# Performance work log

Measured on AMD Instinct MI355X. Metric: run time of the kernel, lower is better.

## Reference

```python
import jax, jax.numpy as jnp
import numpy as np

D_MODEL = 2048; D_STATE = 128; D_CONV = 4; EXPAND = 2
HEADDIM = 64; NGROUPS = 1; CHUNK = 256
D_INNER = EXPAND * D_MODEL          # 4096
NHEADS = D_INNER // HEADDIM         # 64
HG = NHEADS // NGROUPS              # heads per group
CONV_DIM = D_INNER + 2 * NGROUPS * D_STATE          # 4352
D_IN_PROJ = 2 * D_INNER + 2 * NGROUPS * D_STATE + NHEADS  # 8512
BATCH = 2; SEQLEN = 2048
EPS = 1e-5


def setup_inputs() -> dict:
    ks = jax.random.split(jax.random.key(0), 8)
    u = jax.random.normal(ks[0], (BATCH, SEQLEN, D_MODEL), jnp.float32)
    in_proj_w = jax.random.normal(ks[1], (D_IN_PROJ, D_MODEL), jnp.float32) * D_MODEL ** -0.5
    conv_w = jax.random.normal(ks[2], (CONV_DIM, D_CONV), jnp.float32) * D_CONV ** -0.5
    conv_b = jax.random.normal(ks[3], (CONV_DIM,), jnp.float32) * 0.1
    # dt_bias init exactly as in the module: inv softplus of dt ~ U(log(1e-3), log(1e-1))
    dt = jnp.exp(jax.random.uniform(ks[4], (NHEADS,), jnp.float32)
                 * (np.float32(np.log(0.1)) - np.float32(np.log(0.001))) + np.float32(np.log(0.001)))
    dt = jnp.clip(dt, 1e-4, None)
    dt_bias = dt + jnp.log(-jnp.expm1(-dt))
    A_log = jnp.log(jax.random.uniform(ks[5], (NHEADS,), jnp.float32, minval=1.0, maxval=16.0))
    D_skip = jnp.ones((NHEADS,), jnp.float32)
    norm_w = jnp.ones((D_INNER,), jnp.float32)
    out_proj_w = jax.random.normal(ks[6], (D_MODEL, D_INNER), jnp.float32) * D_INNER ** -0.5
    return dict(u=u, in_proj_w=in_proj_w, conv_w=conv_w, conv_b=conv_b,
                dt_bias=dt_bias, A_log=A_log, D_skip=D_skip,
                norm_w=norm_w, out_proj_w=out_proj_w)


def _mamba2(u, in_proj_w, conv_w, conv_b, dt_bias, A_log, D_skip, norm_w, out_proj_w):
    b, l, _ = u.shape
    nc = l // CHUNK
    zxbcdt = u @ in_proj_w.T                                   # (b,l,d_in_proj)
    z = zxbcdt[..., :D_INNER]                                  # gate
    xBC = zxbcdt[..., D_INNER:D_INNER + CONV_DIM]
    dt = jax.nn.softplus(zxbcdt[..., D_INNER + CONV_DIM:] + dt_bias)  # (b,l,h)
    # causal depthwise conv1d (padding d_conv-1, truncated to seqlen) + SiLU
    xp = jnp.pad(xBC, ((0, 0), (D_CONV - 1, 0), (0, 0)))
    conv = conv_b + sum(conv_w[:, k] * xp[:, k:k + l, :] for k in range(D_CONV))
    xBC = jax.nn.silu(conv)
    x = xBC[..., :D_INNER].reshape(b, l, NHEADS, HEADDIM)
    Bm = xBC[..., D_INNER:D_INNER + NGROUPS * D_STATE].reshape(b, l, NGROUPS, D_STATE)
    Cm = xBC[..., D_INNER + NGROUPS * D_STATE:].reshape(b, l, NGROUPS, D_STATE)
    A = -jnp.exp(A_log)                                        # (h,)
    # ---- SSD chunked scan ----
    xc = x.reshape(b, nc, CHUNK, NGROUPS, HG, HEADDIM)         # (b,c,s,g,H,p)
    dtc = dt.reshape(b, nc, CHUNK, NGROUPS, HG)                # (b,c,s,g,H)
    Bc = Bm.reshape(b, nc, CHUNK, NGROUPS, D_STATE)            # (b,c,s,g,n)
    Cc = Cm.reshape(b, nc, CHUNK, NGROUPS, D_STATE)
    dA = jnp.transpose(dtc * A.reshape(NGROUPS, HG), (0, 3, 4, 1, 2))  # (b,g,H,c,s)
    dA_cs = jnp.cumsum(dA, axis=-1)                            # (b,g,H,c,s)
    # intra-chunk: L[i,j] = exp(sum_{j<k<=i} dA_k), lower-triangular (diag=1)
    seg = dA_cs[..., :, None] - dA_cs[..., None, :]            # (b,g,H,c,l,s)
    tri = jnp.tril(jnp.ones((CHUNK, CHUNK), bool))
    Lmat = jnp.where(tri, jnp.exp(seg), 0.0)
    xdt = xc * dtc[..., None]                                  # (b,c,s,g,H,p)
    CB = jnp.einsum('bclgn,bcsgn->bcgls', Cc, Bc)
    Y_diag = jnp.einsum('bcgls,bgHcls,bcsgHp->bclgHp', CB, Lmat, xdt)
    # chunk states and inter-chunk recurrence
    decay_states = jnp.exp(dA_cs[..., -1:] - dA_cs)            # (b,g,H,c,s)
    states = jnp.einsum('bcsgn,bgHcs,bcsgHp->bcgHpn', Bc, decay_states, xdt)
    chunk_decay = jnp.exp(dA_cs[..., -1])                      # (b,g,H,c)

    def step(carry, inp):
        st, dec = inp
        return carry * dec[..., None, None] + st, carry

    _, prev = jax.lax.scan(step, jnp.zeros_like(states[:, 0]),
                           (jnp.moveaxis(states, 1, 0), jnp.moveaxis(chunk_decay, -1, 0)))
    prev = jnp.moveaxis(prev, 0, 1)                            # (b,c,g,H,p,n) state entering chunk
    Y_off = jnp.einsum('bclgn,bcgHpn,bgHcl->bclgHp', Cc, prev, jnp.exp(dA_cs))
    y = (Y_diag + Y_off).reshape(b, l, NHEADS, HEADDIM) + x * D_skip[None, None, :, None]
    y = y.reshape(b, l, D_INNER)
    # gated RMSNorm: gate first (norm_before_gate=False), groupwise rms (ngroups=1 -> full)
    y = y * jax.nn.silu(z)
    yg = y.reshape(b, l, NGROUPS, D_INNER // NGROUPS)
    yg = yg * jax.lax.rsqrt(jnp.mean(yg * yg, axis=-1, keepdims=True) + EPS)
    y = yg.reshape(b, l, D_INNER) * norm_w
    return y @ out_proj_w.T                                    # (b,l,d_model)


def reference(u, in_proj_w, conv_w, conv_b, dt_bias, A_log, D_skip, norm_w, out_proj_w):
    return _mamba2(u, in_proj_w, conv_w, conv_b, dt_bias, A_log, D_skip, norm_w, out_proj_w)
```

## Files before the change

### kernel.cpp

```cpp
#include <hip/hip_runtime.h>
#include <hip/hip_bf16.h>


#define D_MODEL   2048
#define D_STATE   128
#define HEADDIM   64
#define CHUNK     256
#define D_INNER   4096
#define NHEADS    64
#define CONV_DIM  4352
#define D_IN_PROJ 8512
#define SEQLEN    2048
#define NC        8
#define ROWSTOT   4096
#define NPAD      8576
#define RMS_EPS   1e-5f

#define OFF_WIN   0ull
#define OFF_XBF   0ull
#define OFF_PREV  0ull
#define OFF_WOUT  16777216ull
#define OFF_UBF   35127296ull
#define OFF_DTV   35127296ull
#define OFF_DACS  36175872ull
#define OFF_BBF   37224448ull
#define OFF_CBF   38273024ull
#define OFF_CB    39321600ull
#define OFF_BT    43515904ull
#define OFF_XBC   51904512ull
#define OFF_STATE 51904512ull
#define OFF_ZBF   87556096ull
#define OFF_DTRAW 121110528ull
#define OFF_YBUF  121110528ull
#define WS_NEEDED 154664960ull

#define N4_U    2097152l
#define N4_WIN  4390912l

typedef __hip_bfloat16 bf16;
typedef __bf16 bfrag8 __attribute__((ext_vector_type(8)));
typedef float  f32x4v __attribute__((ext_vector_type(4)));

__device__ __forceinline__ f32x4v mfma16(bfrag8 a, bfrag8 b, f32x4v c) {
  return __builtin_amdgcn_mfma_f32_16x16x32_bf16(a, b, c, 0, 0, 0);
}

__device__ __forceinline__ void gload_lds16(const void* g, void* l) {
  __builtin_amdgcn_global_load_lds((const __attribute__((address_space(1))) void*)g,
                                   (__attribute__((address_space(3))) void*)l, 16, 0, 0);
}

__device__ __forceinline__ bf16 f2b(float x) { return __float2bfloat16(x); }
__device__ __forceinline__ float b2f(bf16 x) { return __bfloat162float(x); }
__device__ __forceinline__ float siluf(float x) { return x / (1.f + __expf(-x)); }

__global__ __launch_bounds__(256) void cast_all_kernel(const float* __restrict__ u,
    const float* __restrict__ w_in,
    bf16* __restrict__ u_bf, bf16* __restrict__ win_bf) {
  long i = (long)blockIdx.x * 256 + threadIdx.x;
  if (i < N4_U) {
    float4 v = ((const float4*)u)[i];
    bf16* o = u_bf + i * 4;
    o[0] = f2b(v.x); o[1] = f2b(v.y); o[2] = f2b(v.z); o[3] = f2b(v.w);
  } else if (i < N4_U + N4_WIN) {
    long e = (i - N4_U) * 4;
    long row = e / D_MODEL;
    bf16* o = win_bf + e;
    if (row < D_IN_PROJ) {
      float4 v = *(const float4*)(w_in + e);
      o[0] = f2b(v.x); o[1] = f2b(v.y); o[2] = f2b(v.z); o[3] = f2b(v.w);
    } else {
      bf16 z = f2b(0.f);
      o[0] = z; o[1] = z; o[2] = z; o[3] = z;
    }
  }
}


__global__ __launch_bounds__(512) void gemm1_kernel(const bf16* __restrict__ A,
                                                    const bf16* __restrict__ B,
                                                    bf16* __restrict__ zb,
                                                    bf16* __restrict__ xbc,
                                                    float* __restrict__ dtraw) {
  int pid = blockIdx.x;
  int t = pid & 63, s = pid >> 6;
  int sm = s / 9, sn = s % 9;
  int xcd = t & 7, j8 = t >> 3;
  int tm = sm * 8 + (xcd >> 1) * 2 + (j8 & 1);
  int tn = sn * 8 + (xcd & 1) * 4 + (j8 >> 1);
  if (tn >= 67) return;
  long row0 = (long)tm * 256, col0 = (long)tn * 128;

  __shared__ __align__(16) bf16 As[2 * 256 * 32];
  __shared__ __align__(16) bf16 Bs[2 * 128 * 32];
  int tid = threadIdx.x, lane = tid & 63, w = tid >> 6;
  int wr = w >> 1, wc = w & 1, r16 = lane & 15, q = lane >> 4;
  int qs = (q ^ ((r16 >> 1) & 3)) * 8;
  const int K = D_MODEL;
  f32x4v zero4 = {0.f, 0.f, 0.f, 0.f};
  f32x4v acc[4][4];
#pragma unroll
  for (int i = 0; i < 4; ++i)
#pragma unroll
    for (int j = 0; j < 4; ++j) acc[i][j] = zero4;

  for (int kt = 0; kt < K; kt += 64) {
    __syncthreads();
#pragma unroll
    for (int j = 0; j < 4; ++j) {
      int ci = j * 512 + tid;
      int half = ci >> 10, cj = ci & 1023;
      int r = cj >> 2;
      int ko = half * 32 + ((cj & 3) ^ ((cj >> 3) & 3)) * 8;
      gload_lds16(A + (row0 + r) * (long)K + kt + ko,
                  (char*)As + j * 8192 + w * 1024);
    }
#pragma unroll
    for (int j = 0; j < 2; ++j) {
      int ci = j * 512 + tid;
      int half = ci >> 9, cj = ci & 511;
      int r = cj >> 2;
      int ko = half * 32 + ((cj & 3) ^ ((cj >> 3) & 3)) * 8;
      gload_lds16(B + (col0 + r) * (long)K + kt + ko,
                  (char*)Bs + j * 8192 + w * 1024);
    }
    __syncthreads();
#pragma unroll
    for (int ks = 0; ks < 2; ++ks) {
      const bf16* Ab = As + ks * 8192;
      const bf16* Bb = Bs + ks * 4096;
      bfrag8 af[4], bfv[4];
#pragma unroll
      for (int i = 0; i < 4; ++i) af[i]  = *(const bfrag8*)(Ab + (wr * 64 + i * 16 + r16) * 32 + qs);
#pragma unroll
      for (int i = 0; i < 4; ++i) bfv[i] = *(const bfrag8*)(Bb + (wc * 64 + i * 16 + r16) * 32 + qs);
#pragma unroll
      for (int i = 0; i < 4; ++i)
#pragma unroll
        for (int j = 0; j < 4; ++j) acc[i][j] = mfma16(af[i], bfv[j], acc[i][j]);
    }
  }
#pragma unroll
  for (int i = 0; i < 4; ++i)
#pragma unroll
    for (int j = 0; j < 4; ++j) {
      long col = col0 + wc * 64 + j * 16 + r16;
#pragma unroll
      for (int r = 0; r < 4; ++r) {
        long row = row0 + wr * 64 + i * 16 + q * 4 + r;
        float v = acc[i][j][r];
        if (col < D_INNER)                       zb[row * D_INNER + col] = f2b(v);
        else if (col < D_INNER + CONV_DIM)       xbc[row * CONV_DIM + (col - D_INNER)] = f2b(v);
        else if (col < D_IN_PROJ)                dtraw[row * NHEADS + (col - D_INNER - CONV_DIM)] = v;
      }
    }
}

__global__ __launch_bounds__(256) void gemm2_kernel(const bf16* __restrict__ A,
                                                    const bf16* __restrict__ B,
                                                    float* __restrict__ C) {
  int pid = blockIdx.x;
  int t = pid & 63, s = pid >> 6;
  int sm = s >> 1, sn = s & 1;
  int xcd = t & 7, j8 = t >> 3;
  int tm = sm * 8 + (xcd >> 1) * 2 + (j8 & 1);
  int tn = sn * 8 + (xcd & 1) * 4 + (j8 >> 1);
  long row0 = (long)tm * 128, col0 = (long)tn * 128;

  __shared__ __align__(16) bf16 As[2 * 128 * 32];
  __shared__ __align__(16) bf16 Bs[2 * 128 * 32];
  int tid = threadIdx.x, lane = tid & 63, w = tid >> 6;
  int wr = w >> 1, wc = w & 1, r16 = lane & 15, q = lane >> 4;
  int qs = (q ^ ((r16 >> 1) & 3)) * 8;
  const int K = D_INNER, ldc = D_MODEL;
  f32x4v zero4 = {0.f, 0.f, 0.f, 0.f};
  f32x4v acc[4][4];
#pragma unroll
  for (int i = 0; i < 4; ++i)
#pragma unroll
    for (int j = 0; j < 4; ++j) acc[i][j] = zero4;

  for (int kt = 0; kt < K; kt += 64) {
    __syncthreads();
#pragma unroll
    for (int j = 0; j < 4; ++j) {
      int ci = (j * 4 + w) * 64 + lane;
      int half = ci >> 9, cj = ci & 511;
      int r = cj >> 2;
      int ko = half * 32 + ((cj & 3) ^ ((cj >> 3) & 3)) * 8;
      gload_lds16(A + (row0 + r) * (long)K + kt + ko,
                  (char*)As + (j * 4 + w) * 1024);
    }
#pragma unroll
    for (int j = 0; j < 4; ++j) {
      int ci = (j * 4 + w) * 64 + lane;
      int half = ci >> 9, cj = ci & 511;
      int r = cj >> 2;
      int ko = half * 32 + ((cj & 3) ^ ((cj >> 3) & 3)) * 8;
      gload_lds16(B + (col0 + r) * (long)K + kt + ko,
                  (char*)Bs + (j * 4 + w) * 1024);
    }
    __syncthreads();
#pragma unroll
    for (int ks = 0; ks < 2; ++ks) {
      const bf16* Ab = As + ks * 4096;
      const bf16* Bb = Bs + ks * 4096;
      bfrag8 af[4], bfv[4];
#pragma unroll
      for (int i = 0; i < 4; ++i) af[i]  = *(const bfrag8*)(Ab + (wr * 64 + i * 16 + r16) * 32 + qs);
#pragma unroll
      for (int i = 0; i < 4; ++i) bfv[i] = *(const bfrag8*)(Bb + (wc * 64 + i * 16 + r16) * 32 + qs);
#pragma unroll
      for (int i = 0; i < 4; ++i)
#pragma unroll
        for (int j = 0; j < 4; ++j) acc[i][j] = mfma16(af[i], bfv[j], acc[i][j]);
    }
  }
#pragma unroll
  for (int i = 0; i < 4; ++i)
#pragma unroll
    for (int j = 0; j < 4; ++j)
#pragma unroll
      for (int r = 0; r < 4; ++r) {
        long row = row0 + wr * 64 + i * 16 + q * 4 + r;
        long col = col0 + wc * 64 + j * 16 + r16;
        C[row * ldc + col] = acc[i][j][r];
      }
}

__global__ __launch_bounds__(256) void conv_dt_kernel(
    const float* __restrict__ dtraw, const float* __restrict__ dt_bias,
    const float* __restrict__ A_log, float* __restrict__ dtv_buf,
    float* __restrict__ dacs_buf,
    const bf16* __restrict__ xbc, const float* __restrict__ conv_w,
    const float* __restrict__ conv_b, bf16* __restrict__ xo,
    bf16* __restrict__ Bo, bf16* __restrict__ Co, bf16* __restrict__ BT) {
  if (blockIdx.x < 1024) {
    int blk = blockIdx.x;
    int c = blk & 7, h = (blk >> 3) & 63, b = blk >> 9;
    int s = threadIdx.x, lane = s & 63, w = s >> 6;
    long row = (long)b * SEQLEN + c * CHUNK + s;
    float raw = dtraw[row * NHEADS + h] + dt_bias[h];
    float dtv = fmaxf(raw, 0.f) + log1pf(__expf(-fabsf(raw)));
    float A = -__expf(A_log[h]);
    float x = dtv * A;
#pragma unroll
    for (int off = 1; off < 64; off <<= 1) {
      float y = __shfl_up(x, off);
      if (lane >= off) x += y;
    }
    __shared__ __align__(16) float wsum[4];
    if (lane == 63) wsum[w] = x;
    __syncthreads();
    float pre = 0.f;
#pragma unroll
    for (int i = 0; i < 4; ++i) pre += (i < w) ? wsum[i] : 0.f;
    long o = ((long)(b * NHEADS + h) * NC + c) * CHUNK + s;
    dtv_buf[o] = dtv;
    dacs_buf[o] = x + pre;
    return;
  }
  int t = blockIdx.x - 1024;
  int bx = t % 17;
  int rest = t / 17;
  int by = rest & 255, bz = rest >> 8;
  int cidx = bx * 256 + threadIdx.x;
  int l0 = by * 8, b = bz;
  float4 wv = *(const float4*)(conv_w + cidx * 4);
  float bias = conv_b[cidx];
  const bf16* base = xbc + (long)b * SEQLEN * CONV_DIM + cidx;
  float win[11];
#pragma unroll
  for (int k = 0; k < 11; ++k) {
    int ls = l0 - 3 + k;
    win[k] = (ls >= 0) ? b2f(base[(long)ls * CONV_DIM]) : 0.f;
  }
  int cgrp = (cidx < D_INNER) ? 0 : ((cidx < D_INNER + D_STATE) ? 1 : 2);
  int n = cidx - D_INNER;
  int n2 = cidx - D_INNER - D_STATE;
  int cch = l0 >> 8;
#pragma unroll
  for (int j = 0; j < 8; ++j) {
    float acc = bias + wv.x * win[j] + wv.y * win[j + 1] + wv.z * win[j + 2] + wv.w * win[j + 3];
    bf16 o = f2b(siluf(acc));
    int l = l0 + j;
    long rowo = (long)b * SEQLEN + l;
    if (cgrp == 0) {
      xo[rowo * D_INNER + cidx] = o;
    } else if (cgrp == 1) {
      Bo[rowo * D_STATE + n] = o;
      BT[(((long)b * NC + cch) * D_STATE + n) * CHUNK + (l & 255)] = o;
    } else {
      Co[rowo * D_STATE + n2] = o;
    }
  }
}

__global__ __launch_bounds__(256) void cb_kernel(const bf16* __restrict__ Cg,
                                                 const bf16* __restrict__ Bg,
                                                 float* __restrict__ CB) {
  int blk = blockIdx.x;
  int stile = blk & 3, bc = blk >> 2;
  int c = bc & 7, b = bc >> 3;
  int tid = threadIdx.x, lane = tid & 63, w = tid >> 6, r16 = lane & 15, q = lane >> 4;
  const bf16* Cb = Cg + ((long)b * SEQLEN + c * CHUNK) * D_STATE;
  const bf16* Bb = Bg + ((long)b * SEQLEN + c * CHUNK) * D_STATE;
  bfrag8 af[4][4];
#pragma unroll
  for (int lt = 0; lt < 4; ++lt)
#pragma unroll
    for (int kk = 0; kk < 4; ++kk)
      af[lt][kk] = *(const bfrag8*)(Cb + (long)(w * 64 + lt * 16 + r16) * D_STATE + kk * 32 + q * 8);
  float* CBb = CB + (long)bc * CHUNK * CHUNK;
  f32x4v zero4 = {0.f, 0.f, 0.f, 0.f};
  for (int st = stile * 4; st < stile * 4 + 4; ++st) {
    f32x4v acc[4] = {zero4, zero4, zero4, zero4};
#pragma unroll
    for (int kk = 0; kk < 4; ++kk) {
      bfrag8 bfv = *(const bfrag8*)(Bb + (long)(st * 16 + r16) * D_STATE + kk * 32 + q * 8);
#pragma unroll
      for (int lt = 0; lt < 4; ++lt) acc[lt] = mfma16(af[lt][kk], bfv, acc[lt]);
    }
#pragma unroll
    for (int lt = 0; lt < 4; ++lt)
#pragma unroll
      for (int r = 0; r < 4; ++r)
        CBb[(long)(w * 64 + lt * 16 + q * 4 + r) * CHUNK + st * 16 + r16] = acc[lt][r];
  }
}

__global__ __launch_bounds__(256) void ssm_diag_kernel(
    const bf16* __restrict__ xg, const bf16* __restrict__ BT,
    const float* __restrict__ CB, const float* __restrict__ dtv_buf,
    const float* __restrict__ dacs_buf, const float* __restrict__ Dskip,
    bf16* __restrict__ ybuf, float* __restrict__ states) {
  int blk = blockIdx.x;
  int h = blk & 63, cc = (blk >> 6) & 7, b = blk >> 9;
  int tid = threadIdx.x, lane = tid & 63, w = tid >> 6, r16 = lane & 15, q = lane >> 4;

  __shared__ __align__(16) __bf16 xT[HEADDIM][264];
  __shared__ __align__(16) float cs_s[CHUNK];
  __shared__ __align__(16) float dt_s[CHUNK];
  __shared__ __align__(16) float w_s[CHUNK];

  long hco = ((long)(b * NHEADS + h) * NC + cc) * CHUNK;
  cs_s[tid] = dacs_buf[hco + tid];
  dt_s[tid] = dtv_buf[hco + tid];
  __syncthreads();
  float cl_last = cs_s[CHUNK - 1];
  w_s[tid] = __expf(cl_last - cs_s[tid]) * dt_s[tid];

  const __bf16* xbase = (const __bf16*)(xg + ((long)b * SEQLEN + cc * CHUNK) * D_INNER + h * HEADDIM);
#pragma unroll
  for (int it = 0; it < 8; ++it) {
    int e = it * 256 + tid;
    int s = e >> 3, p0 = (e & 7) * 8;
    bfrag8 xv = *(const bfrag8*)(xbase + (long)s * D_INNER + p0);
#pragma unroll
    for (int j = 0; j < 8; ++j) xT[p0 + j][s] = xv[j];
  }
  __syncthreads();

  const float* CBchunk = CB + (long)(b * NC + cc) * CHUNK * CHUNK;
  const __bf16* BTc = (const __bf16*)(BT + (((long)b * NC + cc) * D_STATE) * CHUNK);
  f32x4v zero4 = {0.f, 0.f, 0.f, 0.f};
  f32x4v accY[4][4], accS[2][4];
#pragma unroll
  for (int i = 0; i < 4; ++i)
#pragma unroll
    for (int j = 0; j < 4; ++j) accY[i][j] = zero4;
#pragma unroll
  for (int i = 0; i < 2; ++i)
#pragma unroll
    for (int j = 0; j < 4; ++j) accS[i][j] = zero4;

  int l_row[4];
  const float* CBrow[4];
#pragma unroll
  for (int lt = 0; lt < 4; ++lt) {
    l_row[lt] = w * 64 + lt * 16 + r16;
    CBrow[lt] = CBchunk + (long)l_row[lt] * CHUNK;
  }

#pragma unroll 2
  for (int ks = 0; ks < 8; ++ks) {
    int s0 = ks * 32 + q * 8;
    float4 cs0 = *(const float4*)(cs_s + s0);
    float4 cs1 = *(const float4*)(cs_s + s0 + 4);
    float4 dt0 = *(const float4*)(dt_s + s0);
    float4 dt1 = *(const float4*)(dt_s + s0 + 4);
    float4 w0  = *(const float4*)(w_s + s0);
    float4 w1  = *(const float4*)(w_s + s0 + 4);
    float csv[8] = {cs0.x, cs0.y, cs0.z, cs0.w, cs1.x, cs1.y, cs1.z, cs1.w};
    float dtv8[8] = {dt0.x, dt0.y, dt0.z, dt0.w, dt1.x, dt1.y, dt1.z, dt1.w};
    float wv8[8]  = {w0.x, w0.y, w0.z, w0.w, w1.x, w1.y, w1.z, w1.w};

    bfrag8 xf[4];
#pragma unroll
    for (int pt = 0; pt < 4; ++pt) xf[pt] = *(const bfrag8*)(&xT[pt * 16 + r16][s0]);

#pragma unroll
    for (int lt = 0; lt < 4; ++lt) {
      int l = l_row[lt];
      float cs_l = cs_s[l];
      float4 cb0 = *(const float4*)(CBrow[lt] + s0);
      float4 cb1 = *(const float4*)(CBrow[lt] + s0 + 4);
      float cbv[8] = {cb0.x, cb0.y, cb0.z, cb0.w, cb1.x, cb1.y, cb1.z, cb1.w};
      bfrag8 pf;
#pragma unroll
      for (int j = 0; j < 8; ++j) {
        float v = (s0 + j <= l)
                    ? cbv[j] * __expf(fminf(cs_l - csv[j], 0.f)) * dtv8[j]
                    : 0.f;
        pf[j] = (__bf16)v;
      }
#pragma unroll
      for (int pt = 0; pt < 4; ++pt) accY[lt][pt] = mfma16(pf, xf[pt], accY[lt][pt]);
    }

#pragma unroll
    for (int nt = 0; nt < 2; ++nt) {
      int n = w * 32 + nt * 16 + r16;
      bfrag8 braw = *(const bfrag8*)(BTc + (long)n * CHUNK + s0);
      bfrag8 bwf;
#pragma unroll
      for (int j = 0; j < 8; ++j) bwf[j] = (__bf16)((float)braw[j] * wv8[j]);
#pragma unroll
      for (int pt = 0; pt < 4; ++pt) accS[nt][pt] = mfma16(bwf, xf[pt], accS[nt][pt]);
    }
  }

  float dsk = Dskip[h];
  bf16* ybase = ybuf + ((long)b * SEQLEN + cc * CHUNK) * D_INNER + h * HEADDIM;
#pragma unroll
  for (int lt = 0; lt < 4; ++lt)
#pragma unroll
    for (int pt = 0; pt < 4; ++pt)
#pragma unroll
      for (int r = 0; r < 4; ++r) {
        int lrow = w * 64 + lt * 16 + q * 4 + r;
        int pcol = pt * 16 + r16;
        ybase[(long)lrow * D_INNER + pcol] = f2b(accY[lt][pt][r] + (float)xT[pcol][lrow] * dsk);
      }
  float* sbase = states + (long)blk * (HEADDIM * D_STATE);
#pragma unroll
  for (int nt = 0; nt < 2; ++nt)
#pragma unroll
    for (int pt = 0; pt < 4; ++pt)
#pragma unroll
      for (int r = 0; r < 4; ++r)
        sbase[(long)(pt * 16 + r16) * D_STATE + w * 32 + nt * 16 + q * 4 + r] = accS[nt][pt][r];
}

__global__ __launch_bounds__(256) void state_scan_kernel(const float* __restrict__ states,
    const float* __restrict__ dacs, bf16* __restrict__ prevb) {
  int gid = blockIdx.x;
  int et = gid & 31, bh = gid >> 5;
  int h = bh & 63, b = bh >> 6;
  int e = et * 256 + threadIdx.x;
  float dec[NC];
#pragma unroll
  for (int c = 0; c < NC; ++c)
    dec[c] = __expf(dacs[((long)(b * NHEADS + h) * NC + c) * CHUNK + (CHUNK - 1)]);
  float carry = 0.f;
#pragma unroll
  for (int c = 0; c < NC; ++c) {
    long off = ((long)((b * NC + c) * NHEADS + h)) * (HEADDIM * D_STATE) + e;
    prevb[off] = f2b(carry);
    carry = carry * dec[c] + states[off];
  }
}

__global__ __launch_bounds__(256) void yoff_kernel(const bf16* __restrict__ Cg,
    const bf16* __restrict__ prevb, const float* __restrict__ dacs,
    bf16* __restrict__ ybuf) {
  int blk = blockIdx.x;
  int h = blk & 63, cc = (blk >> 6) & 7, b = blk >> 9;
  int tid = threadIdx.x, lane = tid & 63, w = tid >> 6, r16 = lane & 15, q = lane >> 4;
  __shared__ __align__(16) float cs_s[CHUNK];
  cs_s[tid] = dacs[((long)(b * NHEADS + h) * NC + cc) * CHUNK + tid];
  __syncthreads();
  const bf16* Cb = Cg + ((long)b * SEQLEN + cc * CHUNK) * D_STATE;
  const bf16* Pb = prevb + (long)blk * (HEADDIM * D_STATE);
  f32x4v zero4 = {0.f, 0.f, 0.f, 0.f};
  f32x4v acc[4][4];
#pragma unroll
  for (int i = 0; i < 4; ++i)
#pragma unroll
    for (int j = 0; j < 4; ++j) acc[i][j] = zero4;
#pragma unroll
  for (int kk = 0; kk < 4; ++kk) {
    bfrag8 bv[4];
#pragma unroll
    for (int pt = 0; pt < 4; ++pt)
      bv[pt] = *(const bfrag8*)(Pb + (long)(pt * 16 + r16) * D_STATE + kk * 32 + q * 8);
#pragma unroll
    for (int lt = 0; lt < 4; ++lt) {
      bfrag8 av = *(const bfrag8*)(Cb + (long)(w * 64 + lt * 16 + r16) * D_STATE + kk * 32 + q * 8);
#pragma unroll
      for (int pt = 0; pt < 4; ++pt) acc[lt][pt] = mfma16(av, bv[pt], acc[lt][pt]);
    }
  }
  bf16* ybase = ybuf + ((long)b * SEQLEN + cc * CHUNK) * D_INNER + h * HEADDIM;
#pragma unroll
  for (int lt = 0; lt < 4; ++lt)
#pragma unroll
    for (int pt = 0; pt < 4; ++pt)
#pragma unroll
      for (int r = 0; r < 4; ++r) {
        int lrow = w * 64 + lt * 16 + q * 4 + r;
        float ef = __expf(cs_s[lrow]);
        bf16* p = ybase + (long)lrow * D_INNER + pt * 16 + r16;
        *p = f2b(b2f(*p) + acc[lt][pt][r] * ef);
      }
}

__global__ __launch_bounds__(256) void cast_gate_kernel(
    const float* __restrict__ w_out, bf16* __restrict__ wout_bf,
    bf16* __restrict__ ybuf, const bf16* __restrict__ zb,
    const float* __restrict__ norm_w) {
  if (blockIdx.x < 8192) {
    long i = (long)blockIdx.x * 256 + threadIdx.x;
    float4 v = ((const float4*)w_out)[i];
    bf16* o = wout_bf + i * 4;
    o[0] = f2b(v.x); o[1] = f2b(v.y); o[2] = f2b(v.z); o[3] = f2b(v.w);
    return;
  }
  int row = blockIdx.x - 8192, tid = threadIdx.x;
  bf16* y = ybuf + (long)row * D_INNER;
  const bf16* z = zb + (long)row * D_INNER;
  float v[16];
  float ss = 0.f;
#pragma unroll
  for (int i = 0; i < 2; ++i) {
    int e = tid * 16 + i * 8;
    bfrag8 yv = *(const bfrag8*)(y + e);
    bfrag8 zv = *(const bfrag8*)(z + e);
#pragma unroll
    for (int j = 0; j < 8; ++j) {
      float a = (float)yv[j] * siluf((float)zv[j]);
      v[i * 8 + j] = a;
      ss += a * a;
    }
  }
#pragma unroll
  for (int off = 32; off > 0; off >>= 1) ss += __shfl_down(ss, off);
  __shared__ __align__(16) float red[4];
  int lane = tid & 63, w = tid >> 6;
  if (lane == 0) red[w] = ss;
  __syncthreads();
  float tot = red[0] + red[1] + red[2] + red[3];
  float scale = rsqrtf(tot * (1.f / D_INNER) + RMS_EPS);
#pragma unroll
  for (int i = 0; i < 2; ++i) {
    int e = tid * 16 + i * 8;
    float4 w0 = *(const float4*)(norm_w + e);
    float4 w1 = *(const float4*)(norm_w + e + 4);
    bfrag8 o;
    o[0] = (__bf16)(v[i * 8 + 0] * scale * w0.x);
    o[1] = (__bf16)(v[i * 8 + 1] * scale * w0.y);
    o[2] = (__bf16)(v[i * 8 + 2] * scale * w0.z);
    o[3] = (__bf16)(v[i * 8 + 3] * scale * w0.w);
    o[4] = (__bf16)(v[i * 8 + 4] * scale * w1.x);
    o[5] = (__bf16)(v[i * 8 + 5] * scale * w1.y);
    o[6] = (__bf16)(v[i * 8 + 6] * scale * w1.z);
    o[7] = (__bf16)(v[i * 8 + 7] * scale * w1.w);
    *(bfrag8*)(y + e) = o;
  }
}

extern "C" void kernel_launch(void* const* d_in, const int* in_sizes, int n_in,
                              void* d_out, int out_size, void* d_ws, size_t ws_size,
                              hipStream_t stream) {
  if (ws_size < WS_NEEDED) return;

  const float* u       = (const float*)d_in[0];
  const float* w_in    = (const float*)d_in[1];
  const float* conv_w  = (const float*)d_in[2];
  const float* conv_b  = (const float*)d_in[3];
  const float* dt_bias = (const float*)d_in[4];
  const float* A_log   = (const float*)d_in[5];
  const float* Dskip   = (const float*)d_in[6];
  const float* norm_w  = (const float*)d_in[7];
  const float* w_out   = (const float*)d_in[8];
  float* out = (float*)d_out;

  char* ws = (char*)d_ws;
  bf16*  win_bf  = (bf16*)(ws + OFF_WIN);
  bf16*  x_bf    = (bf16*)(ws + OFF_XBF);
  bf16*  prevb   = (bf16*)(ws + OFF_PREV);
  bf16*  wout_bf = (bf16*)(ws + OFF_WOUT);
  bf16*  u_bf    = (bf16*)(ws + OFF_UBF);
  float* dtv     = (float*)(ws + OFF_DTV);
  float* dacs    = (float*)(ws + OFF_DACS);
  bf16*  B_bf    = (bf16*)(ws + OFF_BBF);
  bf16*  C_bf    = (bf16*)(ws + OFF_CBF);
  float* CBb     = (float*)(ws + OFF_CB);
  bf16*  BT_bf   = (bf16*)(ws + OFF_BT);
  bf16*  xbc_bf  = (bf16*)(ws + OFF_XBC);
  float* states  = (float*)(ws + OFF_STATE);
  bf16*  z_bf    = (bf16*)(ws + OFF_ZBF);
  float* dt_raw  = (float*)(ws + OFF_DTRAW);
  bf16*  ybuf    = (bf16*)(ws + OFF_YBUF);

  cast_all_kernel<<<25344, 256, 0, stream>>>(u, w_in, u_bf, win_bf);
  gemm1_kernel<<<1152, 512, 0, stream>>>(u_bf, win_bf, z_bf, xbc_bf, dt_raw);
  conv_dt_kernel<<<9728, 256, 0, stream>>>(dt_raw, dt_bias, A_log, dtv, dacs,
                                           xbc_bf, conv_w, conv_b, x_bf, B_bf, C_bf, BT_bf);
  cb_kernel<<<64, 256, 0, stream>>>(C_bf, B_bf, CBb);
  ssm_diag_kernel<<<1024, 256, 0, stream>>>(x_bf, BT_bf, CBb, dtv, dacs, Dskip, ybuf, states);
  state_scan_kernel<<<4096, 256, 0, stream>>>(states, dacs, prevb);
  yoff_kernel<<<1024, 256, 0, stream>>>(C_bf, prevb, dacs, ybuf);
  cast_gate_kernel<<<12288, 256, 0, stream>>>(w_out, wout_bf, ybuf, z_bf, norm_w);
  gemm2_kernel<<<512, 256, 0, stream>>>(ybuf, wout_bf, out);
}
```

Before: 561.2 us.

## Rewrite input-projection GEMM with 256x256 tiles and software-pipelined LDS prefetch

The in_proj GEMM moves from 256x128 tiles with a plain load/sync/compute loop to 256x256 tiles. Each tile is split into four 128-row halves staged through a double-buffered LDS ring, and the next k-tile is prefetched while MFMAs run. It uses inline ds_read_b128, explicit vmcnt waits, raw s_barrier, setprio around the MFMA bursts, and a new XCD-aware block mapping over 544 blocks. The aim is to hide global-load latency and raise arithmetic intensity per block. In exchange it uses more registers and LDS, and depends on fragile hand-written waitcnt ordering.

```diff
diff --git a/kernel.cpp b/kernel.cpp
--- a/kernel.cpp
+++ b/kernel.cpp
@@ -53,6 +53,16 @@
 __device__ __forceinline__ bf16 f2b(float x) { return __float2bfloat16(x); }
 __device__ __forceinline__ float b2f(bf16 x) { return __bfloat162float(x); }
 __device__ __forceinline__ float siluf(float x) { return x / (1.f + __expf(-x)); }
+
+#define BARRIER() asm volatile("s_barrier" ::: "memory")
+#define WAITV(N) asm volatile("s_waitcnt vmcnt(" #N ")" ::: "memory")
+
+__device__ __forceinline__ bfrag8 ds_read_b128f(const bf16* p) {
+  bfrag8 d;
+  unsigned a = (unsigned)(unsigned long long)p;
+  asm volatile("ds_read_b128 %0, %1" : "=&v"(d) : "v"(a));
+  return d;
+}
 
 __global__ __launch_bounds__(256) void cast_all_kernel(const float* __restrict__ u,
     const float* __restrict__ w_in,
@@ -77,78 +87,126 @@
 }
 
 
-__global__ __launch_bounds__(512) void gemm1_kernel(const bf16* __restrict__ A,
-                                                    const bf16* __restrict__ B,
-                                                    bf16* __restrict__ zb,
-                                                    bf16* __restrict__ xbc,
-                                                    float* __restrict__ dtraw) {
+__device__ __forceinline__ void stage_half(const bf16* __restrict__ src,
+    long rowbeg, int rowclamp, int kt, char* lds_slot, int tid, int w) {
+  int r = tid >> 2;
+  int ko0 = ((tid & 3) ^ ((tid >> 3) & 3)) * 8;
+  long row = rowbeg + r;
+  if (row > rowclamp) row = rowclamp;
+  const bf16* g0 = src + row * (long)D_MODEL + kt + ko0;
+  gload_lds16(g0,      lds_slot + w * 1024);
+  gload_lds16(g0 + 32, lds_slot + 8192 + w * 1024);
+}
+
+template<int AS0, int AS1, int WS0, int WS1>
+__device__ __forceinline__ void ktile_bf(
+    const bf16* __restrict__ Ab, const bf16* __restrict__ Bb,
+    const bf16* As, const bf16* Bs, char* AsB, char* BsB,
+    long row0, long col0, int ktpref,
+    int wr16, int wc16, int r16, int qs, int tid, int w,
+    f32x4v (&acc)[8][4], bfrag8 (&bfv)[4][2]) {
+#pragma unroll
+  for (int q = 0; q < 4; ++q) {
+    const bf16* Asl = As + (q < 2 ? AS0 : AS1) * 8192;
+    bfrag8 af[2][2];
+#pragma unroll
+    for (int ii = 0; ii < 2; ++ii) {
+      int rih = (q & 1) * 64 + ii * 32 + wr16 + r16;
+#pragma unroll
+      for (int ks = 0; ks < 2; ++ks)
+        af[ii][ks] = ds_read_b128f(Asl + ks * 4096 + rih * 32 + qs);
+    }
+    if (q == 0) {
+#pragma unroll
+      for (int j = 0; j < 4; ++j) {
+        const bf16* Bsl = Bs + (j < 2 ? AS0 : AS1) * 8192;
+        int rih = (j & 1) * 64 + wc16 + r16;
+#pragma unroll
+        for (int ks = 0; ks < 2; ++ks)
+          bfv[j][ks] = ds_read_b128f(Bsl + ks * 4096 + rih * 32 + qs);
+      }
+      stage_half(Bb, col0,       NPAD - 1, ktpref, BsB + WS0 * 16384, tid, w);
+    } else if (q == 1) {
+      stage_half(Bb, col0 + 128, NPAD - 1, ktpref, BsB + WS1 * 16384, tid, w);
+      WAITV(4);
+    } else if (q == 2) {
+      stage_half(Ab, row0,       ROWSTOT - 1, ktpref, AsB + WS0 * 16384, tid, w);
+    } else {
+      stage_half(Ab, row0 + 128, ROWSTOT - 1, ktpref, AsB + WS1 * 16384, tid, w);
+      WAITV(2);
+    }
+    BARRIER();
+    asm volatile("s_waitcnt lgkmcnt(0)" ::: "memory");
+    __builtin_amdgcn_sched_barrier(0);
+    __builtin_amdgcn_s_setprio(1);
+#pragma unroll
+    for (int ii = 0; ii < 2; ++ii)
+#pragma unroll
+      for (int j = 0; j < 4; ++j) {
+        acc[2 * q + ii][j] = mfma16(af[ii][0], bfv[j][0], acc[2 * q + ii][j]);
+        acc[2 * q + ii][j] = mfma16(af[ii][1], bfv[j][1], acc[2 * q + ii][j]);
+      }
+    __builtin_amdgcn_s_setprio(0);
+    BARRIER();
+  }
+}
+
+__global__ __launch_bounds__(512, 2) void gemm1_kernel(const bf16* __restrict__ A,
+                                                       const bf16* __restrict__ B,
+                                                       bf16* __restrict__ zb,
+                                                       bf16* __restrict__ xbc,
+                                                       float* __restrict__ dtraw) {
   int pid = blockIdx.x;
-  int t = pid & 63, s = pid >> 6;
-  int sm = s / 9, sn = s % 9;
-  int xcd = t & 7, j8 = t >> 3;
-  int tm = sm * 8 + (xcd >> 1) * 2 + (j8 & 1);
-  int tn = sn * 8 + (xcd & 1) * 4 + (j8 >> 1);
-  if (tn >= 67) return;
-  long row0 = (long)tm * 256, col0 = (long)tn * 128;
-
-  __shared__ __align__(16) bf16 As[2 * 256 * 32];
-  __shared__ __align__(16) bf16 Bs[2 * 128 * 32];
+  int xcd = pid & 7, local = pid >> 3;
+  int wgid = xcd * 68 + local;
+  int tm = wgid & 15, tn = wgid >> 4;
+  long row0 = (long)tm * 256, col0 = (long)tn * 256;
+
+  __shared__ __align__(16) bf16 As[4 * 8192];
+  __shared__ __align__(16) bf16 Bs[4 * 8192];
+  char* AsB = (char*)&As[0];
+  char* BsB = (char*)&Bs[0];
+
   int tid = threadIdx.x, lane = tid & 63, w = tid >> 6;
-  int wr = w >> 1, wc = w & 1, r16 = lane & 15, q = lane >> 4;
-  int qs = (q ^ ((r16 >> 1) & 3)) * 8;
-  const int K = D_MODEL;
+  int r16 = lane & 15, qh = lane >> 4;
+  int qs = (qh ^ ((r16 >> 1) & 3)) * 8;
+  int wr16 = (w >> 2) * 16, wc16 = (w & 3) * 16;
+
   f32x4v zero4 = {0.f, 0.f, 0.f, 0.f};
-  f32x4v acc[4][4];
-#pragma unroll
-  for (int i = 0; i < 4; ++i)
+  f32x4v acc[8][4];
+#pragma unroll
+  for (int i = 0; i < 8; ++i)
 #pragma unroll
     for (int j = 0; j < 4; ++j) acc[i][j] = zero4;
-
-  for (int kt = 0; kt < K; kt += 64) {
-    __syncthreads();
+  bfrag8 bfv[4][2];
+
+  stage_half(B, col0,       NPAD - 1,   0, BsB + 0 * 16384, tid, w);
+  stage_half(B, col0 + 128, NPAD - 1,   0, BsB + 1 * 16384, tid, w);
+  stage_half(A, row0,       ROWSTOT - 1, 0, AsB + 0 * 16384, tid, w);
+  stage_half(A, row0 + 128, ROWSTOT - 1, 0, AsB + 1 * 16384, tid, w);
+  WAITV(2);
+  BARRIER();
+
+#pragma unroll 1
+  for (int tt = 0; tt < 16; ++tt) {
+    int k1 = (2 * tt + 1) * 64;
+    int k2 = (tt == 15) ? 31 * 64 : (2 * tt + 2) * 64;
+    ktile_bf<0, 1, 2, 3>(A, B, As, Bs, AsB, BsB, row0, col0, k1,
+                         wr16, wc16, r16, qs, tid, w, acc, bfv);
+    ktile_bf<2, 3, 0, 1>(A, B, As, Bs, AsB, BsB, row0, col0, k2,
+                         wr16, wc16, r16, qs, tid, w, acc, bfv);
+  }
+  WAITV(0);
+
+#pragma unroll
+  for (int i = 0; i < 8; ++i)
 #pragma unroll
     for (int j = 0; j < 4; ++j) {
-      int ci = j * 512 + tid;
-      int half = ci >> 10, cj = ci & 1023;
-      int r = cj >> 2;
-      int ko = half * 32 + ((cj & 3) ^ ((cj >> 3) & 3)) * 8;
-      gload_lds16(A + (row0 + r) * (long)K + kt + ko,
-                  (char*)As + j * 8192 + w * 1024);
-    }
-#pragma unroll
-    for (int j = 0; j < 2; ++j) {
-      int ci = j * 512 + tid;
-      int half = ci >> 9, cj = ci & 511;
-      int r = cj >> 2;
-      int ko = half * 32 + ((cj & 3) ^ ((cj >> 3) & 3)) * 8;
-      gload_lds16(B + (col0 + r) * (long)K + kt + ko,
-                  (char*)Bs + j * 8192 + w * 1024);
-    }
-    __syncthreads();
-#pragma unroll
-    for (int ks = 0; ks < 2; ++ks) {
-      const bf16* Ab = As + ks * 8192;
-      const bf16* Bb = Bs + ks * 4096;
-      bfrag8 af[4], bfv[4];
-#pragma unroll
-      for (int i = 0; i < 4; ++i) af[i]  = *(const bfrag8*)(Ab + (wr * 64 + i * 16 + r16) * 32 + qs);
-#pragma unroll
-      for (int i = 0; i < 4; ++i) bfv[i] = *(const bfrag8*)(Bb + (wc * 64 + i * 16 + r16) * 32 + qs);
-#pragma unroll
-      for (int i = 0; i < 4; ++i)
-#pragma unroll
-        for (int j = 0; j < 4; ++j) acc[i][j] = mfma16(af[i], bfv[j], acc[i][j]);
-    }
-  }
-#pragma unroll
-  for (int i = 0; i < 4; ++i)
-#pragma unroll
-    for (int j = 0; j < 4; ++j) {
-      long col = col0 + wc * 64 + j * 16 + r16;
-#pragma unroll
-      for (int r = 0; r < 4; ++r) {
-        long row = row0 + wr * 64 + i * 16 + q * 4 + r;
-        float v = acc[i][j][r];
+      long col = col0 + j * 64 + wc16 + r16;
+#pragma unroll
+      for (int rr = 0; rr < 4; ++rr) {
+        long row = row0 + i * 32 + wr16 + qh * 4 + rr;
+        float v = acc[i][j][rr];
         if (col < D_INNER)                       zb[row * D_INNER + col] = f2b(v);
         else if (col < D_INNER + CONV_DIM)       xbc[row * CONV_DIM + (col - D_INNER)] = f2b(v);
         else if (col < D_IN_PROJ)                dtraw[row * NHEADS + (col - D_INNER - CONV_DIM)] = v;
@@ -604,7 +662,7 @@
   bf16*  ybuf    = (bf16*)(ws + OFF_YBUF);
 
   cast_all_kernel<<<25344, 256, 0, stream>>>(u, w_in, u_bf, win_bf);
-  gemm1_kernel<<<1152, 512, 0, stream>>>(u_bf, win_bf, z_bf, xbc_bf, dt_raw);
+  gemm1_kernel<<<544, 512, 0, stream>>>(u_bf, win_bf, z_bf, xbc_bf, dt_raw);
   conv_dt_kernel<<<9728, 256, 0, stream>>>(dt_raw, dt_bias, A_log, dtv, dacs,
                                            xbc_bf, conv_w, conv_b, x_bf, B_bf, C_bf, BT_bf);
   cb_kernel<<<64, 256, 0, stream>>>(C_bf, B_bf, CBb);
```

Result: no change. 564.3 us (+0.6%).

## Rewrite out-projection GEMM with 256x128 tiles and triple-buffered async LDS pipeline

Applied to the files above, without the earlier changes.

The output projection GEMM now uses 512-thread blocks computing 256x128 tiles, with a three-stage LDS ring buffer. Global-to-LDS loads for step k+2 are issued while MFMAs run on the current step, using explicit vmcnt waits, raw barriers, inline ds_read_b128 and setprio. The aim is to hide global load latency and cut the per-iteration syncthreads stalls of the old double-sync loop. In exchange it uses more LDS per block and halves the grid to 256 blocks, which may underfill the CUs, and correctness relies on hand-placed waitcnt values.

```diff
diff --git a/kernel.cpp b/kernel.cpp
--- a/kernel.cpp
+++ b/kernel.cpp
@@ -53,6 +53,17 @@
 __device__ __forceinline__ bf16 f2b(float x) { return __float2bfloat16(x); }
 __device__ __forceinline__ float b2f(bf16 x) { return __bfloat162float(x); }
 __device__ __forceinline__ float siluf(float x) { return x / (1.f + __expf(-x)); }
+
+#define BARRIER() asm volatile("s_barrier" ::: "memory")
+#define WAITV(N) asm volatile("s_waitcnt vmcnt(" #N ")" ::: "memory")
+#define LGKM0()  asm volatile("s_waitcnt lgkmcnt(0)" ::: "memory")
+
+__device__ __forceinline__ bfrag8 ds_read_b128f(const bf16* p) {
+  bfrag8 d;
+  unsigned a = (unsigned)(unsigned long long)p;
+  asm volatile("ds_read_b128 %0, %1" : "=&v"(d) : "v"(a));
+  return d;
+}
 
 __global__ __launch_bounds__(256) void cast_all_kernel(const float* __restrict__ u,
     const float* __restrict__ w_in,
@@ -156,23 +167,37 @@
     }
 }
 
-__global__ __launch_bounds__(256) void gemm2_kernel(const bf16* __restrict__ A,
-                                                    const bf16* __restrict__ B,
-                                                    float* __restrict__ C) {
+template<int LD>
+__device__ __forceinline__ void stage_half2(const bf16* __restrict__ src,
+    long rowbeg, int kt, char* lds_slot, int tid, int w) {
+  int r = tid >> 2;
+  int ko0 = ((tid & 3) ^ ((tid >> 3) & 3)) * 8;
+  const bf16* g0 = src + (rowbeg + r) * (long)LD + kt + ko0;
+  gload_lds16(g0,      lds_slot + w * 1024);
+  gload_lds16(g0 + 32, lds_slot + 8192 + w * 1024);
+}
+
+__global__ __launch_bounds__(512, 2) void gemm2_kernel(const bf16* __restrict__ A,
+                                                       const bf16* __restrict__ Bw,
+                                                       float* __restrict__ C) {
   int pid = blockIdx.x;
-  int t = pid & 63, s = pid >> 6;
-  int sm = s >> 1, sn = s & 1;
-  int xcd = t & 7, j8 = t >> 3;
-  int tm = sm * 8 + (xcd >> 1) * 2 + (j8 & 1);
-  int tn = sn * 8 + (xcd & 1) * 4 + (j8 >> 1);
-  long row0 = (long)tm * 128, col0 = (long)tn * 128;
-
-  __shared__ __align__(16) bf16 As[2 * 128 * 32];
-  __shared__ __align__(16) bf16 Bs[2 * 128 * 32];
+  int tn = (pid & 7) * 2 + (pid >> 7);
+  int tm = (pid >> 3) & 15;
+  long row0 = (long)tm * 256, col0 = (long)tn * 128;
+
+  __shared__ __align__(16) bf16 As[6 * 8192];
+  __shared__ __align__(16) bf16 Bs[3 * 8192];
+  char* AsB = (char*)&As[0];
+  char* BsB = (char*)&Bs[0];
+
   int tid = threadIdx.x, lane = tid & 63, w = tid >> 6;
-  int wr = w >> 1, wc = w & 1, r16 = lane & 15, q = lane >> 4;
-  int qs = (q ^ ((r16 >> 1) & 3)) * 8;
-  const int K = D_INNER, ldc = D_MODEL;
+  int r16 = lane & 15, qh = lane >> 4;
+  int qs = (qh ^ ((r16 >> 1) & 3)) * 8;
+  int wm = w >> 1, wn = w & 1;
+  int hsel = wm >> 1;
+  int rih = (wm & 1) * 64 + r16;
+  int cb = wn * 64 + r16;
+
   f32x4v zero4 = {0.f, 0.f, 0.f, 0.f};
   f32x4v acc[4][4];
 #pragma unroll
@@ -180,51 +205,71 @@
 #pragma unroll
     for (int j = 0; j < 4; ++j) acc[i][j] = zero4;
 
-  for (int kt = 0; kt < K; kt += 64) {
-    __syncthreads();
-#pragma unroll
-    for (int j = 0; j < 4; ++j) {
-      int ci = (j * 4 + w) * 64 + lane;
-      int half = ci >> 9, cj = ci & 511;
-      int r = cj >> 2;
-      int ko = half * 32 + ((cj & 3) ^ ((cj >> 3) & 3)) * 8;
-      gload_lds16(A + (row0 + r) * (long)K + kt + ko,
-                  (char*)As + (j * 4 + w) * 1024);
-    }
-#pragma unroll
-    for (int j = 0; j < 4; ++j) {
-      int ci = (j * 4 + w) * 64 + lane;
-      int half = ci >> 9, cj = ci & 511;
-      int r = cj >> 2;
-      int ko = half * 32 + ((cj & 3) ^ ((cj >> 3) & 3)) * 8;
-      gload_lds16(B + (col0 + r) * (long)K + kt + ko,
-                  (char*)Bs + (j * 4 + w) * 1024);
-    }
-    __syncthreads();
-#pragma unroll
-    for (int ks = 0; ks < 2; ++ks) {
-      const bf16* Ab = As + ks * 4096;
-      const bf16* Bb = Bs + ks * 4096;
-      bfrag8 af[4], bfv[4];
-#pragma unroll
-      for (int i = 0; i < 4; ++i) af[i]  = *(const bfrag8*)(Ab + (wr * 64 + i * 16 + r16) * 32 + qs);
-#pragma unroll
-      for (int i = 0; i < 4; ++i) bfv[i] = *(const bfrag8*)(Bb + (wc * 64 + i * 16 + r16) * 32 + qs);
-#pragma unroll
-      for (int i = 0; i < 4; ++i)
-#pragma unroll
-        for (int j = 0; j < 4; ++j) acc[i][j] = mfma16(af[i], bfv[j], acc[i][j]);
-    }
-  }
+  stage_half2<D_INNER>(A,  row0,       0,  AsB + 0 * 16384, tid, w);
+  stage_half2<D_INNER>(Bw, col0,       0,  BsB + 0 * 16384, tid, w);
+  stage_half2<D_INNER>(A,  row0 + 128, 0,  AsB + 1 * 16384, tid, w);
+  stage_half2<D_INNER>(A,  row0,       64, AsB + 2 * 16384, tid, w);
+  stage_half2<D_INNER>(Bw, col0,       64, BsB + 1 * 16384, tid, w);
+  stage_half2<D_INNER>(A,  row0 + 128, 64, AsB + 3 * 16384, tid, w);
+  WAITV(6);
+  BARRIER();
+
+  int cur = 0, pf = 2;
+#pragma unroll 1
+  for (int tt = 0; tt < 64; ++tt) {
+    int kpref = (tt < 62 ? tt + 2 : 63) * 64;
+    const bf16* Asl = As + (cur * 2 + hsel) * 8192;
+    const bf16* Bsl = Bs + cur * 8192;
+    bfrag8 af[4], bfv[4];
+
+#pragma unroll
+    for (int i = 0; i < 4; ++i) af[i]  = ds_read_b128f(Asl + (rih + i * 16) * 32 + qs);
+#pragma unroll
+    for (int j = 0; j < 4; ++j) bfv[j] = ds_read_b128f(Bsl + (cb + j * 16) * 32 + qs);
+    stage_half2<D_INNER>(A,  row0,       kpref, AsB + (pf * 2) * 16384, tid, w);
+    stage_half2<D_INNER>(Bw, col0,       kpref, BsB + pf * 16384, tid, w);
+    BARRIER();
+    LGKM0();
+    __builtin_amdgcn_sched_barrier(0);
+    __builtin_amdgcn_s_setprio(1);
+#pragma unroll
+    for (int i = 0; i < 4; ++i)
+#pragma unroll
+      for (int j = 0; j < 4; ++j) acc[i][j] = mfma16(af[i], bfv[j], acc[i][j]);
+    __builtin_amdgcn_s_setprio(0);
+    BARRIER();
+
+#pragma unroll
+    for (int i = 0; i < 4; ++i) af[i]  = ds_read_b128f(Asl + 4096 + (rih + i * 16) * 32 + qs);
+#pragma unroll
+    for (int j = 0; j < 4; ++j) bfv[j] = ds_read_b128f(Bsl + 4096 + (cb + j * 16) * 32 + qs);
+    stage_half2<D_INNER>(A,  row0 + 128, kpref, AsB + (pf * 2 + 1) * 16384, tid, w);
+    WAITV(6);
+    BARRIER();
+    LGKM0();
+    __builtin_amdgcn_sched_barrier(0);
+    __builtin_amdgcn_s_setprio(1);
+#pragma unroll
+    for (int i = 0; i < 4; ++i)
+#pragma unroll
+      for (int j = 0; j < 4; ++j) acc[i][j] = mfma16(af[i], bfv[j], acc[i][j]);
+    __builtin_amdgcn_s_setprio(0);
+    BARRIER();
+
+    cur = (cur == 2) ? 0 : cur + 1;
+    pf  = (pf  == 2) ? 0 : pf + 1;
+  }
+  WAITV(0);
+
 #pragma unroll
   for (int i = 0; i < 4; ++i)
 #pragma unroll
     for (int j = 0; j < 4; ++j)
 #pragma unroll
       for (int r = 0; r < 4; ++r) {
-        long row = row0 + wr * 64 + i * 16 + q * 4 + r;
-        long col = col0 + wc * 64 + j * 16 + r16;
-        C[row * ldc + col] = acc[i][j][r];
+        long row = row0 + wm * 64 + i * 16 + qh * 4 + r;
+        long col = col0 + wn * 64 + j * 16 + r16;
+        C[row * (long)D_MODEL + col] = acc[i][j][r];
       }
 }
 
@@ -612,5 +657,5 @@
   state_scan_kernel<<<4096, 256, 0, stream>>>(states, dacs, prevb);
   yoff_kernel<<<1024, 256, 0, stream>>>(C_bf, prevb, dacs, ybuf);
   cast_gate_kernel<<<12288, 256, 0, stream>>>(w_out, wout_bf, ybuf, z_bf, norm_w);
-  gemm2_kernel<<<512, 256, 0, stream>>>(ybuf, wout_bf, out);
-}
+  gemm2_kernel<<<256, 512, 0, stream>>>(ybuf, wout_bf, out);
+}
```

New measurement: 551.9 us. About the same (-1.6%).
